# Kernel optimization log

Measured on AMD Instinct MI355X. Metric: run time of the kernel, lower is better.

The kernel has to match this reference:

```python
import jax, jax.numpy as jnp
import numpy as np

HEADS = 8
DIM_HEAD = 64


def setup_inputs() -> dict:
    key = jax.random.key(0)
    ks = jax.random.split(key, 6)
    b, n, d = 4, 2048, 512
    inner = HEADS * DIM_HEAD  # 512
    return {
        "x": jax.random.normal(ks[0], (b, n, d), dtype=jnp.float32),
        "W_v": jax.random.normal(ks[1], (d, inner), dtype=jnp.float32) * 0.02,
        "W_sigma": jax.random.normal(ks[2], (d, HEADS), dtype=jnp.float32) * 0.02,
        "b_sigma": jax.random.normal(ks[3], (HEADS,), dtype=jnp.float32) * 0.02,
        "W_out": jax.random.normal(ks[4], (inner, d), dtype=jnp.float32) * 0.02,
        "b_out": jax.random.normal(ks[5], (d,), dtype=jnp.float32) * 0.02,
    }


def reference(x, W_v, W_sigma, b_sigma, W_out, b_out):
    b, n, d = x.shape
    h, dh = HEADS, DIM_HEAD
    # |i - j| distance matrix (linspace(1,n,n) differences == arange differences)
    pos = jnp.arange(n, dtype=x.dtype)
    dist = jnp.abs(pos[:, None] - pos[None, :])  # (n, n)
    # per-query-row sigma: (b, h, n)
    sigma = jax.nn.sigmoid(jnp.einsum("bnd,dh->bhn", x, W_sigma) + b_sigma[None, :, None])
    denom = jnp.exp(sigma) + 1.0  # (b, h, n)
    # prior[b,h,i,j] = softmax_j( -|i-j| / (exp(sigma[b,h,i]) + 1) )
    prior = jax.nn.softmax(-dist[None, None, :, :] / denom[..., None], axis=-1)  # (b,h,n,n)
    v = (x @ W_v).reshape(b, n, h, dh).transpose(0, 2, 1, 3)  # (b,h,n,dh)
    out = jnp.einsum("bhij,bhjd->bhid", prior, v)  # (b,h,n,dh)
    out = out.transpose(0, 2, 1, 3).reshape(b, n, h * dh)
    return out @ W_out + b_out
```

## Files before the change

### kernel.cpp

```cpp
#include <hip/hip_runtime.h>
#include <hip/hip_bf16.h>

#define B 4
#define N 2048
#define D 512
#define H 8
#define DH 64
#define ROWS (B * N)
#define WIN 64
#define LPAD 64
#define RPAD 128
#define SEG (LPAD + N + RPAD)
#define LDV (B * SEG)

using bf16x8 = __attribute__((ext_vector_type(8))) short;
using f32x4  = __attribute__((ext_vector_type(4))) float;

static __device__ __forceinline__ unsigned short f2bf(float f) {
    unsigned u = __builtin_bit_cast(unsigned, f);
    u += 0x7fffu + ((u >> 16) & 1u);
    return (unsigned short)(u >> 16);
}
static __device__ __forceinline__ unsigned pack2(float a, float b) {
    return (unsigned)f2bf(a) | ((unsigned)f2bf(b) << 16);
}

__global__ __launch_bounds__(256) void prep_x(const float* __restrict__ x,
                                              const float* __restrict__ Ws,
                                              const float* __restrict__ bs,
                                              unsigned short* __restrict__ xbf,
                                              float* __restrict__ l2rbuf) {
    const int wid = threadIdx.x >> 6, lane = threadIdx.x & 63;
    const int row = blockIdx.x * 4 + wid;
    const float* xr = x + (size_t)row * D + lane * 8;
    const float4 a = *reinterpret_cast<const float4*>(xr);
    const float4 c = *reinterpret_cast<const float4*>(xr + 4);
    float v[8] = {a.x, a.y, a.z, a.w, c.x, c.y, c.z, c.w};

    uint4 o;
    o.x = pack2(v[0], v[1]); o.y = pack2(v[2], v[3]);
    o.z = pack2(v[4], v[5]); o.w = pack2(v[6], v[7]);
    *reinterpret_cast<uint4*>(xbf + (size_t)row * D + lane * 8) = o;

    const float4* Ws4 = reinterpret_cast<const float4*>(Ws);
    f32x4 alo = (f32x4)0.0f, ahi = (f32x4)0.0f;
#pragma unroll
    for (int j = 0; j < 8; j++) {
        const int e = lane * 8 + j;
        const float4 wl = Ws4[e * 2], wh = Ws4[e * 2 + 1];
        alo[0] += v[j] * wl.x; alo[1] += v[j] * wl.y; alo[2] += v[j] * wl.z; alo[3] += v[j] * wl.w;
        ahi[0] += v[j] * wh.x; ahi[1] += v[j] * wh.y; ahi[2] += v[j] * wh.z; ahi[3] += v[j] * wh.w;
    }
#pragma unroll
    for (int off = 1; off < 64; off <<= 1) {
#pragma unroll
        for (int c2 = 0; c2 < 4; c2++) {
            alo[c2] += __shfl_xor(alo[c2], off, 64);
            ahi[c2] += __shfl_xor(ahi[c2], off, 64);
        }
    }
    if (lane < 8) {
        const int h = lane;
        const float acc = (h < 4) ? alo[h] : ahi[h - 4];
        const float z = acc + bs[h];
        const float sig = 1.0f / (1.0f + expf(-z));
        const float s = expf(sig) + 1.0f;
        l2rbuf[(size_t)row * H + h] = -1.4426950408889634f / s;
    }
}

__global__ __launch_bounds__(256) void transpose_cvt(const float* __restrict__ Wv,
                                                     const float* __restrict__ Wo,
                                                     unsigned short* __restrict__ WvT,
                                                     unsigned short* __restrict__ WoT,
                                                     unsigned short* __restrict__ Vt) {
    if (blockIdx.z == 2) {
        const int blk = blockIdx.x + 8 * blockIdx.y;
        for (int t = blk * 256 + threadIdx.x; t < 512 * 4 * 24; t += 64 * 256) {
            const int c = t % 24;
            const int bb = (t / 24) & 3;
            const int row = t / 96;
            const int col = (c < 8) ? bb * SEG + c * 8 : bb * SEG + LPAD + N + (c - 8) * 8;
            *reinterpret_cast<uint4*>(Vt + (size_t)row * LDV + col) = uint4{0, 0, 0, 0};
        }
        return;
    }
    const float* src = blockIdx.z ? Wo : Wv;
    unsigned short* dst = blockIdx.z ? WoT : WvT;
    __shared__ float tile[64][65];
    const int n0 = blockIdx.x * 64, k0 = blockIdx.y * 64;
    const int tr = threadIdx.x >> 4, tc = threadIdx.x & 15;
#pragma unroll
    for (int it = 0; it < 4; it++) {
        const int r = it * 16 + tr;
        const float4 v = *reinterpret_cast<const float4*>(&src[(size_t)(k0 + r) * 512 + n0 + tc * 4]);
        tile[r][tc * 4 + 0] = v.x; tile[r][tc * 4 + 1] = v.y;
        tile[r][tc * 4 + 2] = v.z; tile[r][tc * 4 + 3] = v.w;
    }
    __syncthreads();
#pragma unroll
    for (int it = 0; it < 4; it++) {
        const int r = it * 16 + tr;
        ushort4 o;
        o.x = f2bf(tile[tc * 4 + 0][r]); o.y = f2bf(tile[tc * 4 + 1][r]);
        o.z = f2bf(tile[tc * 4 + 2][r]); o.w = f2bf(tile[tc * 4 + 3][r]);
        *reinterpret_cast<ushort4*>(&dst[(size_t)(n0 + r) * 512 + k0 + tc * 4]) = o;
    }
}

#define GBM 128
#define GBN 64
#define GBK 64

template <int MODE>
__global__ __launch_bounds__(256) void gemm_bf16(const unsigned short* __restrict__ A,
                                                 const unsigned short* __restrict__ Bt,
                                                 const float* __restrict__ bias,
                                                 void* __restrict__ Cout,
                                                 int M, int Nn, int K, int ldc) {
    __shared__ unsigned short As[2][GBM][GBK];
    __shared__ unsigned short Bs[2][GBN][GBK];
    const int tid = threadIdx.x;
    const int lane = tid & 63, wid = tid >> 6;
    const int wr = wid >> 1, wc = wid & 1;
    const int bm = blockIdx.y, bn = blockIdx.x;
    const int fr = lane & 15, kg = lane >> 4;

    f32x4 acc[4][2] = {};

    const unsigned short* Ab = A + (size_t)bm * GBM * K;
    const unsigned short* Bb = Bt + (size_t)bn * GBN * K;
    const int r8 = tid >> 3, c8 = (tid & 7) * 8;

    auto stage = [&](int buf, int k0) {
#pragma unroll
        for (int it = 0; it < 4; it++) {
            const unsigned short* g = Ab + (size_t)(it * 32 + r8) * K + k0 + c8;
            __builtin_amdgcn_global_load_lds(
                (const __attribute__((address_space(1))) void*)g,
                (__attribute__((address_space(3))) void*)&As[buf][it * 32 + r8][c8], 16, 0, 0);
        }
#pragma unroll
        for (int it = 0; it < 2; it++) {
            const unsigned short* g = Bb + (size_t)(it * 32 + r8) * K + k0 + c8;
            __builtin_amdgcn_global_load_lds(
                (const __attribute__((address_space(1))) void*)g,
                (__attribute__((address_space(3))) void*)&Bs[buf][it * 32 + r8][c8], 16, 0, 0);
        }
    };

    stage(0, 0);
    __syncthreads();
    int cur = 0;
    for (int k0 = 0; k0 < K; k0 += GBK) {
        if (k0 + GBK < K) stage(cur ^ 1, k0 + GBK);
#pragma unroll
        for (int ks = 0; ks < 2; ks++) {
            bf16x8 af[4], bfr[2];
#pragma unroll
            for (int m = 0; m < 4; m++)
                af[m] = *reinterpret_cast<const bf16x8*>(&As[cur][wr * 64 + m * 16 + fr][ks * 32 + kg * 8]);
#pragma unroll
            for (int n = 0; n < 2; n++)
                bfr[n] = *reinterpret_cast<const bf16x8*>(&Bs[cur][wc * 32 + n * 16 + fr][ks * 32 + kg * 8]);
#pragma unroll
            for (int m = 0; m < 4; m++)
#pragma unroll
                for (int n = 0; n < 2; n++)
                    acc[m][n] = __builtin_amdgcn_mfma_f32_16x16x32_bf16(af[m], bfr[n], acc[m][n], 0, 0, 0);
        }
        __syncthreads();
        cur ^= 1;
    }

#pragma unroll
    for (int n = 0; n < 2; n++) {
        const int col = bn * GBN + wc * 32 + n * 16 + fr;
        const float bv = (MODE == 0 && bias) ? bias[col] : 0.0f;
        const int cp = (MODE == 2) ? ((col >> 11) * SEG + LPAD + (col & 2047)) : col;
#pragma unroll
        for (int m = 0; m < 4; m++) {
            const int row0 = bm * GBM + wr * 64 + m * 16 + kg * 4;
#pragma unroll
            for (int j = 0; j < 4; j++) {
                const int row = row0 + j;
                if (MODE == 0)
                    ((float*)Cout)[(size_t)row * ldc + col] = acc[m][n][j] + bv;
                else
                    ((unsigned short*)Cout)[(size_t)row * ldc + cp] = f2bf(acc[m][n][j]);
            }
        }
    }
}

__global__ __launch_bounds__(256) void attn_mfma(const unsigned short* __restrict__ Vt,
                                                 const float* __restrict__ l2rbuf,
                                                 unsigned short* __restrict__ O) {
    const int wid = threadIdx.x >> 6;
    const int lane = threadIdx.x & 63;
    const int fr = lane & 15, kg = lane >> 4;
    const int gi = blockIdx.x * 4 + wid;
    const int iblk = gi & 127;
    const int bh = gi >> 7;
    const int h = bh & 7;
    const int b = bh >> 3;
    const int i0 = iblk * 16;

    const int i = i0 + fr;
    const float l2rf = l2rbuf[((size_t)(b * N + i)) * H + h];

    const unsigned short* Vrow = Vt + (size_t)(h * DH + fr) * LDV + (size_t)b * SEG + i0 + kg * 8;

    f32x4 acc[4] = {};

#pragma unroll
    for (int s = 0; s < 5; s++) {
        const float basef = (float)(s * 32 + kg * 8 - WIN - fr);
        float wv[8];
#pragma unroll
        for (int j2 = 0; j2 < 8; j2++)
            wv[j2] = __builtin_amdgcn_exp2f(l2rf * __builtin_fabsf(basef + (float)j2));
        uint4 uw;
        uw.x = pack2(wv[0], wv[1]); uw.y = pack2(wv[2], wv[3]);
        uw.z = pack2(wv[4], wv[5]); uw.w = pack2(wv[6], wv[7]);
        const bf16x8 pB = __builtin_bit_cast(bf16x8, uw);
#pragma unroll
        for (int sub = 0; sub < 4; sub++) {
            const bf16x8 aF = *reinterpret_cast<const bf16x8*>(Vrow + (size_t)(sub * 16) * LDV + s * 32);
            acc[sub] = __builtin_amdgcn_mfma_f32_16x16x32_bf16(aF, pB, acc[sub], 0, 0, 0);
        }
    }

    const float rr = __builtin_amdgcn_exp2f(l2rf);
    const float inv1mr = 1.0f / (1.0f - rr);
    const float rl = __builtin_amdgcn_exp2f(l2rf * (float)(i + 1));
    const float rg = __builtin_amdgcn_exp2f(l2rf * (float)(N - i));
    const float invz = 1.0f / (1.0f + (2.0f * rr - rl - rg) * inv1mr);

    unsigned short* orow = O + ((size_t)(b * N + i)) * D + h * DH + kg * 4;
#pragma unroll
    for (int sub = 0; sub < 4; sub++) {
        uint2 o;
        o.x = pack2(acc[sub][0] * invz, acc[sub][1] * invz);
        o.y = pack2(acc[sub][2] * invz, acc[sub][3] * invz);
        *reinterpret_cast<uint2*>(orow + sub * 16) = o;
    }
}

extern "C" void kernel_launch(void* const* d_in, const int* in_sizes, int n_in,
                              void* d_out, int out_size, void* d_ws, size_t ws_size,
                              hipStream_t stream) {
    const float* x      = (const float*)d_in[0];
    const float* W_v    = (const float*)d_in[1];
    const float* W_sig  = (const float*)d_in[2];
    const float* b_sig  = (const float*)d_in[3];
    const float* W_out  = (const float*)d_in[4];
    const float* b_out  = (const float*)d_in[5];
    float* out = (float*)d_out;

    char* ws = (char*)d_ws;
    unsigned short* Vt   = (unsigned short*)ws;
    unsigned short* xbf  = (unsigned short*)(ws + (size_t)9  * 1024 * 1024);
    unsigned short* WvT  = (unsigned short*)(ws + (size_t)17 * 1024 * 1024);
    unsigned short* WoT  = (unsigned short*)(ws + (size_t)17 * 1024 * 1024 + 524288);
    float*          l2r  = (float*)(ws + (size_t)18 * 1024 * 1024);
    unsigned short* attnOut = xbf;

    prep_x<<<ROWS / 4, 256, 0, stream>>>(x, W_sig, b_sig, xbf, l2r);
    {
        dim3 grid(8, 8, 3);
        transpose_cvt<<<grid, 256, 0, stream>>>(W_v, W_out, WvT, WoT, Vt);
    }

    {
        dim3 grid(ROWS / GBN, 512 / GBM);
        gemm_bf16<2><<<grid, 256, 0, stream>>>(WvT, xbf, nullptr, Vt, 512, ROWS, D, LDV);
    }
    attn_mfma<<<B * H * (N / 16) / 4, 256, 0, stream>>>(Vt, l2r, attnOut);
    {
        dim3 grid(D / GBN, ROWS / GBM);
        gemm_bf16<0><<<grid, 256, 0, stream>>>(attnOut, WoT, b_out, out, ROWS, D, D, D);
    }
}
```

Before: 69.43 us.

## Fuse prep and transpose kernels into one launch; widen GEMM N-tile

Merges the x-conversion/sigma kernel and the weight-transpose/padding-zero kernel into a single launch, dispatching work by block index, which removes one kernel launch and its serialization gap. Separately, it doubles the GEMM block N-tile from 64 to 128, so each wave computes a 64x64 sub-tile with 16 accumulators instead of 8. Larger tiles improve MFMA reuse of LDS fragments but halve the grid size and raise register pressure, which may lower occupancy for the small 512-wide GEMMs.

```diff
diff --git a/kernel.cpp b/kernel.cpp
--- a/kernel.cpp
+++ b/kernel.cpp
@@ -25,91 +25,101 @@
     return (unsigned)f2bf(a) | ((unsigned)f2bf(b) << 16);
 }
 
-__global__ __launch_bounds__(256) void prep_x(const float* __restrict__ x,
-                                              const float* __restrict__ Ws,
-                                              const float* __restrict__ bs,
-                                              unsigned short* __restrict__ xbf,
-                                              float* __restrict__ l2rbuf) {
-    const int wid = threadIdx.x >> 6, lane = threadIdx.x & 63;
-    const int row = blockIdx.x * 4 + wid;
-    const float* xr = x + (size_t)row * D + lane * 8;
-    const float4 a = *reinterpret_cast<const float4*>(xr);
-    const float4 c = *reinterpret_cast<const float4*>(xr + 4);
-    float v[8] = {a.x, a.y, a.z, a.w, c.x, c.y, c.z, c.w};
-
-    uint4 o;
-    o.x = pack2(v[0], v[1]); o.y = pack2(v[2], v[3]);
-    o.z = pack2(v[4], v[5]); o.w = pack2(v[6], v[7]);
-    *reinterpret_cast<uint4*>(xbf + (size_t)row * D + lane * 8) = o;
-
-    const float4* Ws4 = reinterpret_cast<const float4*>(Ws);
-    f32x4 alo = (f32x4)0.0f, ahi = (f32x4)0.0f;
-#pragma unroll
-    for (int j = 0; j < 8; j++) {
-        const int e = lane * 8 + j;
-        const float4 wl = Ws4[e * 2], wh = Ws4[e * 2 + 1];
-        alo[0] += v[j] * wl.x; alo[1] += v[j] * wl.y; alo[2] += v[j] * wl.z; alo[3] += v[j] * wl.w;
-        ahi[0] += v[j] * wh.x; ahi[1] += v[j] * wh.y; ahi[2] += v[j] * wh.z; ahi[3] += v[j] * wh.w;
-    }
-#pragma unroll
-    for (int off = 1; off < 64; off <<= 1) {
-#pragma unroll
-        for (int c2 = 0; c2 < 4; c2++) {
-            alo[c2] += __shfl_xor(alo[c2], off, 64);
-            ahi[c2] += __shfl_xor(ahi[c2], off, 64);
-        }
-    }
-    if (lane < 8) {
-        const int h = lane;
-        const float acc = (h < 4) ? alo[h] : ahi[h - 4];
-        const float z = acc + bs[h];
-        const float sig = 1.0f / (1.0f + expf(-z));
-        const float s = expf(sig) + 1.0f;
-        l2rbuf[(size_t)row * H + h] = -1.4426950408889634f / s;
-    }
-}
-
-__global__ __launch_bounds__(256) void transpose_cvt(const float* __restrict__ Wv,
-                                                     const float* __restrict__ Wo,
-                                                     unsigned short* __restrict__ WvT,
-                                                     unsigned short* __restrict__ WoT,
-                                                     unsigned short* __restrict__ Vt) {
-    if (blockIdx.z == 2) {
-        const int blk = blockIdx.x + 8 * blockIdx.y;
-        for (int t = blk * 256 + threadIdx.x; t < 512 * 4 * 24; t += 64 * 256) {
+__global__ __launch_bounds__(256) void prep_fused(const float* __restrict__ x,
+                                                  const float* __restrict__ Ws,
+                                                  const float* __restrict__ bs,
+                                                  const float* __restrict__ Wv,
+                                                  const float* __restrict__ Wo,
+                                                  unsigned short* __restrict__ xbf,
+                                                  float* __restrict__ l2rbuf,
+                                                  unsigned short* __restrict__ WvT,
+                                                  unsigned short* __restrict__ WoT,
+                                                  unsigned short* __restrict__ Vt) {
+    __shared__ float tile[64][65];
+    const int bx = blockIdx.x;
+
+    if (bx < 2048) {
+        const int wid = threadIdx.x >> 6, lane = threadIdx.x & 63;
+        const int row = bx * 4 + wid;
+        const float* xr = x + (size_t)row * D + lane * 8;
+        const float4 a = *reinterpret_cast<const float4*>(xr);
+        const float4 c = *reinterpret_cast<const float4*>(xr + 4);
+        float v[8] = {a.x, a.y, a.z, a.w, c.x, c.y, c.z, c.w};
+
+        uint4 o;
+        o.x = pack2(v[0], v[1]); o.y = pack2(v[2], v[3]);
+        o.z = pack2(v[4], v[5]); o.w = pack2(v[6], v[7]);
+        *reinterpret_cast<uint4*>(xbf + (size_t)row * D + lane * 8) = o;
+
+        const float4* Ws4 = reinterpret_cast<const float4*>(Ws);
+        f32x4 alo = (f32x4)0.0f, ahi = (f32x4)0.0f;
+#pragma unroll
+        for (int j = 0; j < 8; j++) {
+            const int e = lane * 8 + j;
+            const float4 wl = Ws4[e * 2], wh = Ws4[e * 2 + 1];
+            alo[0] += v[j] * wl.x; alo[1] += v[j] * wl.y; alo[2] += v[j] * wl.z; alo[3] += v[j] * wl.w;
+            ahi[0] += v[j] * wh.x; ahi[1] += v[j] * wh.y; ahi[2] += v[j] * wh.z; ahi[3] += v[j] * wh.w;
+        }
+#pragma unroll
+        for (int off = 1; off < 64; off <<= 1) {
+#pragma unroll
+            for (int c2 = 0; c2 < 4; c2++) {
+                alo[c2] += __shfl_xor(alo[c2], off, 64);
+                ahi[c2] += __shfl_xor(ahi[c2], off, 64);
+            }
+        }
+        if (lane < 8) {
+            const int h = lane;
+            const float acc = (h < 4) ? alo[h] : ahi[h - 4];
+            const float z = acc + bs[h];
+            const float sig = 1.0f / (1.0f + expf(-z));
+            const float s = expf(sig) + 1.0f;
+            l2rbuf[(size_t)row * H + h] = -1.4426950408889634f / s;
+        }
+        return;
+    }
+
+    if (bx < 2176) {
+        const int idx = bx - 2048;
+        const bool second = idx >= 64;
+        const int id2 = idx & 63;
+        const float* src = second ? Wo : Wv;
+        unsigned short* dst = second ? WoT : WvT;
+        const int n0 = (id2 & 7) * 64, k0 = (id2 >> 3) * 64;
+        const int tr = threadIdx.x >> 4, tc = threadIdx.x & 15;
+#pragma unroll
+        for (int it = 0; it < 4; it++) {
+            const int r = it * 16 + tr;
+            const float4 v = *reinterpret_cast<const float4*>(&src[(size_t)(k0 + r) * 512 + n0 + tc * 4]);
+            tile[r][tc * 4 + 0] = v.x; tile[r][tc * 4 + 1] = v.y;
+            tile[r][tc * 4 + 2] = v.z; tile[r][tc * 4 + 3] = v.w;
+        }
+        __syncthreads();
+#pragma unroll
+        for (int it = 0; it < 4; it++) {
+            const int r = it * 16 + tr;
+            ushort4 o;
+            o.x = f2bf(tile[tc * 4 + 0][r]); o.y = f2bf(tile[tc * 4 + 1][r]);
+            o.z = f2bf(tile[tc * 4 + 2][r]); o.w = f2bf(tile[tc * 4 + 3][r]);
+            *reinterpret_cast<ushort4*>(&dst[(size_t)(n0 + r) * 512 + k0 + tc * 4]) = o;
+        }
+        return;
+    }
+
+    {
+        const int idx = bx - 2176;
+        for (int t = idx * 256 + threadIdx.x; t < 512 * 4 * 24; t += 64 * 256) {
             const int c = t % 24;
             const int bb = (t / 24) & 3;
             const int row = t / 96;
             const int col = (c < 8) ? bb * SEG + c * 8 : bb * SEG + LPAD + N + (c - 8) * 8;
             *reinterpret_cast<uint4*>(Vt + (size_t)row * LDV + col) = uint4{0, 0, 0, 0};
         }
-        return;
-    }
-    const float* src = blockIdx.z ? Wo : Wv;
-    unsigned short* dst = blockIdx.z ? WoT : WvT;
-    __shared__ float tile[64][65];
-    const int n0 = blockIdx.x * 64, k0 = blockIdx.y * 64;
-    const int tr = threadIdx.x >> 4, tc = threadIdx.x & 15;
-#pragma unroll
-    for (int it = 0; it < 4; it++) {
-        const int r = it * 16 + tr;
-        const float4 v = *reinterpret_cast<const float4*>(&src[(size_t)(k0 + r) * 512 + n0 + tc * 4]);
-        tile[r][tc * 4 + 0] = v.x; tile[r][tc * 4 + 1] = v.y;
-        tile[r][tc * 4 + 2] = v.z; tile[r][tc * 4 + 3] = v.w;
-    }
-    __syncthreads();
-#pragma unroll
-    for (int it = 0; it < 4; it++) {
-        const int r = it * 16 + tr;
-        ushort4 o;
-        o.x = f2bf(tile[tc * 4 + 0][r]); o.y = f2bf(tile[tc * 4 + 1][r]);
-        o.z = f2bf(tile[tc * 4 + 2][r]); o.w = f2bf(tile[tc * 4 + 3][r]);
-        *reinterpret_cast<ushort4*>(&dst[(size_t)(n0 + r) * 512 + k0 + tc * 4]) = o;
     }
 }
 
 #define GBM 128
-#define GBN 64
+#define GBN 128
 #define GBK 64
 
 template <int MODE>
@@ -126,7 +136,7 @@
     const int bm = blockIdx.y, bn = blockIdx.x;
     const int fr = lane & 15, kg = lane >> 4;
 
-    f32x4 acc[4][2] = {};
+    f32x4 acc[4][4] = {};
 
     const unsigned short* Ab = A + (size_t)bm * GBM * K;
     const unsigned short* Bb = Bt + (size_t)bn * GBN * K;
@@ -141,7 +151,7 @@
                 (__attribute__((address_space(3))) void*)&As[buf][it * 32 + r8][c8], 16, 0, 0);
         }
 #pragma unroll
-        for (int it = 0; it < 2; it++) {
+        for (int it = 0; it < 4; it++) {
             const unsigned short* g = Bb + (size_t)(it * 32 + r8) * K + k0 + c8;
             __builtin_amdgcn_global_load_lds(
                 (const __attribute__((address_space(1))) void*)g,
@@ -156,17 +166,17 @@
         if (k0 + GBK < K) stage(cur ^ 1, k0 + GBK);
 #pragma unroll
         for (int ks = 0; ks < 2; ks++) {
-            bf16x8 af[4], bfr[2];
+            bf16x8 af[4], bfr[4];
 #pragma unroll
             for (int m = 0; m < 4; m++)
                 af[m] = *reinterpret_cast<const bf16x8*>(&As[cur][wr * 64 + m * 16 + fr][ks * 32 + kg * 8]);
 #pragma unroll
-            for (int n = 0; n < 2; n++)
-                bfr[n] = *reinterpret_cast<const bf16x8*>(&Bs[cur][wc * 32 + n * 16 + fr][ks * 32 + kg * 8]);
+            for (int n = 0; n < 4; n++)
+                bfr[n] = *reinterpret_cast<const bf16x8*>(&Bs[cur][wc * 64 + n * 16 + fr][ks * 32 + kg * 8]);
 #pragma unroll
             for (int m = 0; m < 4; m++)
 #pragma unroll
-                for (int n = 0; n < 2; n++)
+                for (int n = 0; n < 4; n++)
                     acc[m][n] = __builtin_amdgcn_mfma_f32_16x16x32_bf16(af[m], bfr[n], acc[m][n], 0, 0, 0);
         }
         __syncthreads();
@@ -174,8 +184,8 @@
     }
 
 #pragma unroll
-    for (int n = 0; n < 2; n++) {
-        const int col = bn * GBN + wc * 32 + n * 16 + fr;
+    for (int n = 0; n < 4; n++) {
+        const int col = bn * GBN + wc * 64 + n * 16 + fr;
         const float bv = (MODE == 0 && bias) ? bias[col] : 0.0f;
         const int cp = (MODE == 2) ? ((col >> 11) * SEG + LPAD + (col & 2047)) : col;
 #pragma unroll
@@ -266,11 +276,8 @@
     float*          l2r  = (float*)(ws + (size_t)18 * 1024 * 1024);
     unsigned short* attnOut = xbf;
 
-    prep_x<<<ROWS / 4, 256, 0, stream>>>(x, W_sig, b_sig, xbf, l2r);
-    {
-        dim3 grid(8, 8, 3);
-        transpose_cvt<<<grid, 256, 0, stream>>>(W_v, W_out, WvT, WoT, Vt);
-    }
+    prep_fused<<<2240, 256, 0, stream>>>(x, W_sig, b_sig, W_v, W_out,
+                                         xbf, l2r, WvT, WoT, Vt);
 
     {
         dim3 grid(ROWS / GBN, 512 / GBM);
```

After: 68.13 us. Within noise of the previous version (-1.9%).
